# Performance work log

Hardware: AMD Instinct MI355X
Metric: run time of the kernel (lower is better)

Reference implementation:

```python
import jax, jax.numpy as jnp
import numpy as np

B, S, H = 64, 2048, 512


def _xavier(key, shape):
    fan_in, fan_out = shape[-1], shape[-2] if len(shape) > 1 else 1
    limit = float(np.sqrt(6.0 / (fan_in + fan_out)))
    return jax.random.uniform(key, shape, jnp.float32, -limit, limit)


def setup_inputs() -> dict:
    key = jax.random.key(0)
    k1, k2, k3, k4, k5, k6 = jax.random.split(key, 6)
    keys_ = jax.random.normal(k1, (B, S, H), jnp.float32)
    query = jax.random.normal(k2, (B, H), jnp.float32)
    v1 = _xavier(k3, (H,))
    W1 = _xavier(k4, (H, 2 * H))
    v2 = _xavier(k5, (H,))
    W2 = _xavier(k6, (H, 2 * H))
    return {"keys": keys_, "query": query, "v1": v1, "W1": W1, "v2": v2, "W2": W2}


def reference(keys, query, v1, W1, v2, W2):
    b, s, h = keys.shape
    # Stage 1: additive (Bahdanau) scoring over concat(keys, broadcast query)
    q = jnp.broadcast_to(query[:, None, :], (b, s, h))          # [B,S,H]
    hidden = jnp.concatenate([keys, q], axis=2)                  # [B,S,2H]
    t1 = jnp.tanh(jnp.einsum('de,bse->bsd', W1, hidden))         # [B,S,H]
    scores = jnp.einsum('d,bsd->bs', v1, t1)                     # [B,S]
    attns = jax.nn.softmax(scores, axis=1)                       # [B,S]
    # values == keys in the original module
    new_q = jnp.einsum('bs,bsh->bh', attns, keys)                # [B,H]
    # Stage 2: score again against concat(keys, broadcast new_query)
    nq = jnp.broadcast_to(new_q[:, None, :], (b, s, h))
    hidden2 = jnp.concatenate([keys, nq], axis=2)                # [B,S,2H]
    t2 = jnp.tanh(jnp.einsum('de,bse->bsd', W2, hidden2))        # [B,S,H]
    attn_vecs = jnp.einsum('d,bsd->bs', v2, t2)[:, None, :]      # [B,1,S]
    return attn_vecs
```

## Files before the change

kernel.cpp:

```cpp
#include <hip/hip_runtime.h>
#include <cstdint>
#include <cstddef>

#define S_DIM 2048

typedef __attribute__((ext_vector_type(8))) short short8;
typedef __attribute__((ext_vector_type(4))) float f32x4;

static __device__ __forceinline__ unsigned short f2bf(float f) {
  union { float f; unsigned int u; } v; v.f = f;
  unsigned int r = (v.u + 0x7fffu + ((v.u >> 16) & 1u)) >> 16;
  return (unsigned short)r;
}

static __device__ __forceinline__ float bf2f(unsigned short u) {
  union { unsigned int u; float f; } v; v.u = ((unsigned int)u) << 16;
  return v.f;
}

static __device__ __forceinline__ float fast_tanh(float x) {
  x = fminf(15.f, fmaxf(-15.f, x));
  float e = __expf(x + x);
  return 1.f - 2.f * __builtin_amdgcn_rcpf(e + 1.f);
}

static __device__ __forceinline__ void gload_lds16(const void* g, void* l) {
  __builtin_amdgcn_global_load_lds(
      (const __attribute__((address_space(1))) void*)g,
      (__attribute__((address_space(3))) void*)l, 16, 0, 0);
}


__global__ __launch_bounds__(256) void pack_a_kernel(
    const float* __restrict__ keys, unsigned short* __restrict__ akp) {
  int gid = blockIdx.x * 256 + threadIdx.x;
  int tile = gid >> 12;
  int wt = gid & 4095;
  int k0 = wt >> 8, mr = (wt >> 6) & 3, lhi = (wt >> 4) & 3, l15 = wt & 15;
  const float* src = keys + (size_t)(tile * 64 + mr * 16 + l15) * 512 + k0 * 32 + lhi * 8;
  float4 f0 = *reinterpret_cast<const float4*>(src);
  float4 f1 = *reinterpret_cast<const float4*>(src + 4);
  short8 hv;
  hv[0] = (short)f2bf(f0.x); hv[1] = (short)f2bf(f0.y);
  hv[2] = (short)f2bf(f0.z); hv[3] = (short)f2bf(f0.w);
  hv[4] = (short)f2bf(f1.x); hv[5] = (short)f2bf(f1.y);
  hv[6] = (short)f2bf(f1.z); hv[7] = (short)f2bf(f1.w);
  *reinterpret_cast<short8*>(akp + (size_t)gid * 8) = hv;
}

__global__ __launch_bounds__(256) void pack_b_kernel(
    const float* __restrict__ W1, const float* __restrict__ W2,
    unsigned short* __restrict__ wkp1, unsigned short* __restrict__ wkp2) {
  int j = blockIdx.x * 256 + threadIdx.x;
  const float* W = (j < 32768) ? W1 : W2;
  unsigned short* o = (j < 32768) ? wkp1 : wkp2;
  int wt = j & 32767;
  int k0 = wt >> 11, g = (wt >> 6) & 31, lhi = (wt >> 4) & 3, l15 = wt & 15;
  const float* src = W + (size_t)(g * 16 + l15) * 1024 + k0 * 32 + lhi * 8;
  float4 f0 = *reinterpret_cast<const float4*>(src);
  float4 f1 = *reinterpret_cast<const float4*>(src + 4);
  short8 hv;
  hv[0] = (short)f2bf(f0.x); hv[1] = (short)f2bf(f0.y);
  hv[2] = (short)f2bf(f0.z); hv[3] = (short)f2bf(f0.w);
  hv[4] = (short)f2bf(f1.x); hv[5] = (short)f2bf(f1.y);
  hv[6] = (short)f2bf(f1.z); hv[7] = (short)f2bf(f1.w);
  *reinterpret_cast<short8*>(o + (size_t)wt * 8) = hv;
}

__global__ __launch_bounds__(512, 4) void fused_packed_kernel(
    const unsigned short* __restrict__ akp, const unsigned short* __restrict__ wkp,
    const float* __restrict__ v, const float* __restrict__ qp,
    float* __restrict__ out) {
  __shared__ __align__(16) unsigned short lds_a[32768];
  __shared__ float lds_score[8][64];

  const int tid  = threadIdx.x;
  const int wid  = tid >> 6;
  const int lane = tid & 63;
  const int l15  = lane & 15;
  const int lhi  = lane >> 4;
  const int tile = blockIdx.x;
  const int row0 = tile * 64;
  const int b    = row0 >> 11;
  const int wcol = wid * 64;

  const unsigned short* atile = akp + (size_t)tile * 32768;
  #pragma unroll
  for (int i = 0; i < 8; ++i)
    gload_lds16(atile + (i * 512 + tid) * 8, (char*)lds_a + (i * 512 + tid) * 16);

  const unsigned short* wbase = wkp + (size_t)wid * 2048 + (size_t)lane * 8;
  short8 bb[2][4];
  #pragma unroll
  for (int nc = 0; nc < 4; ++nc)
    bb[0][nc] = *reinterpret_cast<const short8*>(wbase + nc * 512);

  __syncthreads();

  f32x4 acc[4][4];
  #pragma unroll
  for (int mr = 0; mr < 4; ++mr)
    #pragma unroll
    for (int nc = 0; nc < 4; ++nc) {
      f32x4 z = {0.f, 0.f, 0.f, 0.f};
      acc[mr][nc] = z;
    }

  const char* abase = (const char*)lds_a + lane * 16;

  #pragma unroll
  for (int k0 = 0; k0 < 16; ++k0) {
    const int cur = k0 & 1, nxt = cur ^ 1;
    if (k0 < 15) {
      #pragma unroll
      for (int nc = 0; nc < 4; ++nc)
        bb[nxt][nc] = *reinterpret_cast<const short8*>(
            wbase + (size_t)(k0 + 1) * 16384 + nc * 512);
    }
    short8 a[4];
    #pragma unroll
    for (int mr = 0; mr < 4; ++mr)
      a[mr] = *reinterpret_cast<const short8*>(abase + k0 * 4096 + mr * 1024);
    #pragma unroll
    for (int mr = 0; mr < 4; ++mr)
      #pragma unroll
      for (int nc = 0; nc < 4; ++nc)
        acc[mr][nc] = __builtin_amdgcn_mfma_f32_16x16x32_bf16(
            a[mr], bb[cur][nc], acc[mr][nc], 0, 0, 0);
  }

  float rp[4][4];
  #pragma unroll
  for (int mr = 0; mr < 4; ++mr)
    #pragma unroll
    for (int j = 0; j < 4; ++j) rp[mr][j] = 0.f;

  #pragma unroll
  for (int nc = 0; nc < 4; ++nc) {
    int col = wcol + nc * 16 + l15;
    float vv = v[col];
    float qv = qp[b * 512 + col];
    #pragma unroll
    for (int mr = 0; mr < 4; ++mr)
      #pragma unroll
      for (int j = 0; j < 4; ++j)
        rp[mr][j] += fast_tanh(acc[mr][nc][j] + qv) * vv;
  }

  #pragma unroll
  for (int off = 1; off < 16; off <<= 1)
    #pragma unroll
    for (int mr = 0; mr < 4; ++mr)
      #pragma unroll
      for (int j = 0; j < 4; ++j)
        rp[mr][j] += __shfl_xor(rp[mr][j], off, 64);

  if (l15 == 0) {
    #pragma unroll
    for (int mr = 0; mr < 4; ++mr)
      #pragma unroll
      for (int j = 0; j < 4; ++j)
        lds_score[wid][mr * 16 + lhi * 4 + j] = rp[mr][j];
  }
  __syncthreads();
  if (tid < 64) {
    float s = 0.f;
    #pragma unroll
    for (int w = 0; w < 8; ++w) s += lds_score[w][tid];
    out[row0 + tid] = s;
  }
}

__global__ __launch_bounds__(256) void wsum_packed_kernel(
    const unsigned short* __restrict__ akp, const float* __restrict__ attn,
    float* __restrict__ new_q) {
  int b = blockIdx.x, k0 = blockIdx.y;
  int t = threadIdx.x;
  int mr = t >> 6, lhi = (t >> 4) & 3, l15 = t & 15;
  const unsigned short* base =
      akp + (size_t)b * 32 * 32768 + (size_t)k0 * 2048 + (size_t)t * 8;
  const float* ab = attn + b * S_DIM + mr * 16 + l15;
  float acc[8];
  #pragma unroll
  for (int e = 0; e < 8; ++e) acc[e] = 0.f;
  #pragma unroll 4
  for (int tile = 0; tile < 32; ++tile) {
    short8 kv = *reinterpret_cast<const short8*>(base + (size_t)tile * 32768);
    float w = ab[tile * 64];
    #pragma unroll
    for (int e = 0; e < 8; ++e)
      acc[e] += w * bf2f((unsigned short)kv[e]);
  }
  __shared__ float red[4][64][8];
  #pragma unroll
  for (int e = 0; e < 8; ++e) red[lhi][mr * 16 + l15][e] = acc[e];
  __syncthreads();
  if (t < 32) {
    int lh = t >> 3, e = t & 7;
    float s = 0.f;
    #pragma unroll 8
    for (int r = 0; r < 64; ++r) s += red[lh][r][e];
    new_q[b * 512 + k0 * 32 + lh * 8 + e] = s;
  }
}


__global__ __launch_bounds__(512) void qproj_kernel(
    const float* __restrict__ W, const float* __restrict__ x,
    float* __restrict__ qp) {
  __shared__ float xs[512];
  int b = blockIdx.x, d = threadIdx.x;
  xs[d] = x[b * 512 + d];
  __syncthreads();
  const float4* wr = (const float4*)(W + (size_t)d * 1024 + 512);
  const float4* xv = (const float4*)xs;
  float acc = 0.f;
  #pragma unroll 8
  for (int h = 0; h < 128; ++h) {
    float4 w4 = wr[h], x4 = xv[h];
    acc += w4.x * x4.x + w4.y * x4.y + w4.z * x4.z + w4.w * x4.w;
  }
  qp[b * 512 + d] = acc;
}

__global__ __launch_bounds__(256) void softmax_kernel(float* __restrict__ sc) {
  int b = blockIdx.x, tid = threadIdx.x;
  float* row = sc + (size_t)b * S_DIM;
  float vv[8];
  float m = -1e30f;
  #pragma unroll
  for (int i = 0; i < 8; ++i) { vv[i] = row[tid + i * 256]; m = fmaxf(m, vv[i]); }
  #pragma unroll
  for (int off = 32; off; off >>= 1) m = fmaxf(m, __shfl_xor(m, off, 64));
  __shared__ float red[4], red2[4];
  int wid = tid >> 6, lane = tid & 63;
  if (lane == 0) red[wid] = m;
  __syncthreads();
  m = fmaxf(fmaxf(red[0], red[1]), fmaxf(red[2], red[3]));
  float s = 0.f;
  #pragma unroll
  for (int i = 0; i < 8; ++i) { vv[i] = __expf(vv[i] - m); s += vv[i]; }
  #pragma unroll
  for (int off = 32; off; off >>= 1) s += __shfl_xor(s, off, 64);
  if (lane == 0) red2[wid] = s;
  __syncthreads();
  s = red2[0] + red2[1] + red2[2] + red2[3];
  float inv = 1.f / s;
  #pragma unroll
  for (int i = 0; i < 8; ++i) row[tid + i * 256] = vv[i] * inv;
}


__global__ __launch_bounds__(256) void convw_kernel(
    const float* __restrict__ W1, const float* __restrict__ W2,
    unsigned short* __restrict__ wk1, unsigned short* __restrict__ wk2) {
  int idx = blockIdx.x * 256 + threadIdx.x;
  const float* W = (idx < 262144) ? W1 : W2;
  unsigned short* o = (idx < 262144) ? wk1 : wk2;
  int j = idx & 262143;
  int d = j >> 9, h = j & 511;
  o[j] = f2bf(W[(size_t)d * 1024 + h]);
}

__global__ __launch_bounds__(512, 4) void fused_scores_kernel(
    const float* __restrict__ keys, const unsigned short* __restrict__ wk,
    const float* __restrict__ v, const float* __restrict__ qp,
    float* __restrict__ out) {
  __shared__ __align__(16) unsigned short lds_k[64 * 512];
  __shared__ float lds_score[8][64];
  char* lds_b = (char*)lds_k;
  const int tid  = threadIdx.x;
  const int wid  = tid >> 6;
  const int lane = tid & 63;
  const int l15  = lane & 15;
  const int lhi  = lane >> 4;
  const int row0 = blockIdx.x * 64;
  const int b    = row0 >> 11;
  const int wcol = wid * 64;
  #pragma unroll
  for (int i = 0; i < 8; ++i) {
    int c = i * 512 + tid;
    int r = c >> 6, k = (c & 63) * 8;
    const float* src = keys + (size_t)(row0 + r) * 512 + k;
    const float4 f0 = *reinterpret_cast<const float4*>(src);
    const float4 f1 = *reinterpret_cast<const float4*>(src + 4);
    short8 hv;
    hv[0] = (short)f2bf(f0.x); hv[1] = (short)f2bf(f0.y);
    hv[2] = (short)f2bf(f0.z); hv[3] = (short)f2bf(f0.w);
    hv[4] = (short)f2bf(f1.x); hv[5] = (short)f2bf(f1.y);
    hv[6] = (short)f2bf(f1.z); hv[7] = (short)f2bf(f1.w);
    int byte = (r * 1024 + k * 2) ^ ((r & 7) << 4);
    *reinterpret_cast<short8*>(lds_b + byte) = hv;
  }
  __syncthreads();
  f32x4 acc[4][4];
  #pragma unroll
  for (int mr = 0; mr < 4; ++mr)
    #pragma unroll
    for (int nc = 0; nc < 4; ++nc) {
      f32x4 z = {0.f, 0.f, 0.f, 0.f};
      acc[mr][nc] = z;
    }
  const int koff = lhi * 8;
  #pragma unroll 1
  for (int k0 = 0; k0 < 512; k0 += 32) {
    short8 a[4], bbv[4];
    #pragma unroll
    for (int nc = 0; nc < 4; ++nc) {
      const unsigned short* p =
          wk + (((size_t)(wcol + nc * 16 + l15)) << 9) + k0 + koff;
      bbv[nc] = *reinterpret_cast<const short8*>(p);
    }
    #pragma unroll
    for (int mr = 0; mr < 4; ++mr) {
      int r = mr * 16 + l15;
      int byte = (r * 1024 + (k0 + koff) * 2) ^ ((r & 7) << 4);
      a[mr] = *reinterpret_cast<const short8*>(lds_b + byte);
    }
    #pragma unroll
    for (int mr = 0; mr < 4; ++mr)
      #pragma unroll
      for (int nc = 0; nc < 4; ++nc)
        acc[mr][nc] = __builtin_amdgcn_mfma_f32_16x16x32_bf16(
            a[mr], bbv[nc], acc[mr][nc], 0, 0, 0);
  }
  float rp[4][4];
  #pragma unroll
  for (int mr = 0; mr < 4; ++mr)
    #pragma unroll
    for (int j = 0; j < 4; ++j) rp[mr][j] = 0.f;
  #pragma unroll
  for (int nc = 0; nc < 4; ++nc) {
    int col = wcol + nc * 16 + l15;
    float vv = v[col];
    float qv = qp[b * 512 + col];
    #pragma unroll
    for (int mr = 0; mr < 4; ++mr)
      #pragma unroll
      for (int j = 0; j < 4; ++j)
        rp[mr][j] += fast_tanh(acc[mr][nc][j] + qv) * vv;
  }
  #pragma unroll
  for (int off = 1; off < 16; off <<= 1)
    #pragma unroll
    for (int mr = 0; mr < 4; ++mr)
      #pragma unroll
      for (int j = 0; j < 4; ++j)
        rp[mr][j] += __shfl_xor(rp[mr][j], off, 64);
  if (l15 == 0) {
    #pragma unroll
    for (int mr = 0; mr < 4; ++mr)
      #pragma unroll
      for (int j = 0; j < 4; ++j)
        lds_score[wid][mr * 16 + lhi * 4 + j] = rp[mr][j];
  }
  __syncthreads();
  if (tid < 64) {
    float s = 0.f;
    #pragma unroll
    for (int w = 0; w < 8; ++w) s += lds_score[w][tid];
    out[row0 + tid] = s;
  }
}

__global__ __launch_bounds__(512) void wsum_part_kernel(
    const float* __restrict__ keys, const float* __restrict__ attn,
    float* __restrict__ part) {
  int b = blockIdx.x, sc = blockIdx.y;
  int tid = threadIdx.x;
  int c4 = tid & 127, rg = tid >> 7;
  const float* kb = keys + ((size_t)(b * S_DIM + sc * 128 + rg * 32)) * 512 + c4 * 4;
  const float* ab = attn + b * S_DIM + sc * 128 + rg * 32;
  float4 acc = {0.f, 0.f, 0.f, 0.f};
  #pragma unroll 8
  for (int i = 0; i < 32; ++i) {
    float w = ab[i];
    float4 kv = *reinterpret_cast<const float4*>(kb + (size_t)i * 512);
    acc.x += w * kv.x; acc.y += w * kv.y; acc.z += w * kv.z; acc.w += w * kv.w;
  }
  __shared__ float4 red[4][128];
  red[rg][c4] = acc;
  __syncthreads();
  if (tid < 128) {
    float4 a0 = red[0][tid], a1 = red[1][tid], a2 = red[2][tid], a3 = red[3][tid];
    float4 s;
    s.x = a0.x + a1.x + a2.x + a3.x;
    s.y = a0.y + a1.y + a2.y + a3.y;
    s.z = a0.z + a1.z + a2.z + a3.z;
    s.w = a0.w + a1.w + a2.w + a3.w;
    *reinterpret_cast<float4*>(part + ((size_t)b * 16 + sc) * 512 + tid * 4) = s;
  }
}

__global__ __launch_bounds__(512) void wsum_final_kernel(
    const float* __restrict__ part, float* __restrict__ new_q) {
  int b = blockIdx.x, h = threadIdx.x;
  float acc = 0.f;
  #pragma unroll
  for (int sc = 0; sc < 16; ++sc) acc += part[((size_t)b * 16 + sc) * 512 + h];
  new_q[b * 512 + h] = acc;
}


extern "C" void kernel_launch(void* const* d_in, const int* in_sizes, int n_in,
                              void* d_out, int out_size, void* d_ws, size_t ws_size,
                              hipStream_t stream) {
  (void)in_sizes; (void)n_in; (void)out_size;
  const float* keys  = (const float*)d_in[0];
  const float* query = (const float*)d_in[1];
  const float* v1    = (const float*)d_in[2];
  const float* W1    = (const float*)d_in[3];
  const float* v2    = (const float*)d_in[4];
  const float* W2    = (const float*)d_in[5];
  float* out = (float*)d_out;
  float* wsf = (float*)d_ws;

  const size_t FAST_NEED = 491520ull * 4ull + 67108864ull * 2ull;
  if (ws_size >= FAST_NEED) {
    float* qp1   = wsf;
    float* attn  = wsf + 32768;
    float* new_q = wsf + 163840;
    float* qp2   = wsf + 196608;
    unsigned short* wkp1 = (unsigned short*)(wsf + 229376);
    unsigned short* wkp2 = wkp1 + 262144;
    unsigned short* akp  = (unsigned short*)(wsf + 491520);

    pack_a_kernel<<<32768, 256, 0, stream>>>(keys, akp);
    pack_b_kernel<<<256, 256, 0, stream>>>(W1, W2, wkp1, wkp2);
    qproj_kernel<<<64, 512, 0, stream>>>(W1, query, qp1);
    fused_packed_kernel<<<2048, 512, 0, stream>>>(akp, wkp1, v1, qp1, attn);
    softmax_kernel<<<64, 256, 0, stream>>>(attn);
    wsum_packed_kernel<<<dim3(64, 16), 256, 0, stream>>>(akp, attn, new_q);
    qproj_kernel<<<64, 512, 0, stream>>>(W2, new_q, qp2);
    fused_packed_kernel<<<2048, 512, 0, stream>>>(akp, wkp2, v2, qp2, out);
  } else {
    float* qp1   = wsf;
    float* attn  = wsf + 32768;
    float* new_q = wsf + 163840;
    float* qp2   = wsf + 196608;
    float* part  = wsf + 229376;
    unsigned short* wk1 = (unsigned short*)(wsf + 753664);
    unsigned short* wk2 = wk1 + 262144;

    convw_kernel<<<2048, 256, 0, stream>>>(W1, W2, wk1, wk2);
    qproj_kernel<<<64, 512, 0, stream>>>(W1, query, qp1);
    fused_scores_kernel<<<2048, 512, 0, stream>>>(keys, wk1, v1, qp1, attn);
    softmax_kernel<<<64, 256, 0, stream>>>(attn);
    wsum_part_kernel<<<dim3(64, 16), 512, 0, stream>>>(keys, attn, part);
    wsum_final_kernel<<<64, 512, 0, stream>>>(part, new_q);
    qproj_kernel<<<64, 512, 0, stream>>>(W2, new_q, qp2);
    fused_scores_kernel<<<2048, 512, 0, stream>>>(keys, wk2, v2, qp2, out);
  }
}
```

Before: 305.0 us.

## Fuse both key projections into one persistent kernel, defer query-dependent tanh

The key half of the W2 projection does not depend on the new query, so a single persistent kernel now computes keys·W1ᵀ and keys·W2ᵀ together. It stages fp32 keys through double-buffered, XOR-swizzled LDS and converts them to bf16 in registers, which removes the separate key packing pass. The W2 partial products are stored as bf16 and a light finisher kernel later adds the projected new query, applies tanh and the v2 dot product. This saves a second full read of keys and a second GEMM, at the cost of writing and rereading a 128 MB bf16 intermediate, using fp32 keys for the weighted sum, and adding some rounding from the bf16 intermediate.

```diff
diff --git a/kernel.cpp b/kernel.cpp
--- a/kernel.cpp
+++ b/kernel.cpp
@@ -18,6 +18,12 @@
   return v.f;
 }
 
+static __device__ __forceinline__ unsigned int cvt_pk_bf16(float lo, float hi) {
+  unsigned int r;
+  asm("v_cvt_pk_bf16_f32 %0, %1, %2" : "=v"(r) : "v"(lo), "v"(hi));
+  return r;
+}
+
 static __device__ __forceinline__ float fast_tanh(float x) {
   x = fminf(15.f, fmaxf(-15.f, x));
   float e = __expf(x + x);
@@ -28,24 +34,6 @@
   __builtin_amdgcn_global_load_lds(
       (const __attribute__((address_space(1))) void*)g,
       (__attribute__((address_space(3))) void*)l, 16, 0, 0);
-}
-
-
-__global__ __launch_bounds__(256) void pack_a_kernel(
-    const float* __restrict__ keys, unsigned short* __restrict__ akp) {
-  int gid = blockIdx.x * 256 + threadIdx.x;
-  int tile = gid >> 12;
-  int wt = gid & 4095;
-  int k0 = wt >> 8, mr = (wt >> 6) & 3, lhi = (wt >> 4) & 3, l15 = wt & 15;
-  const float* src = keys + (size_t)(tile * 64 + mr * 16 + l15) * 512 + k0 * 32 + lhi * 8;
-  float4 f0 = *reinterpret_cast<const float4*>(src);
-  float4 f1 = *reinterpret_cast<const float4*>(src + 4);
-  short8 hv;
-  hv[0] = (short)f2bf(f0.x); hv[1] = (short)f2bf(f0.y);
-  hv[2] = (short)f2bf(f0.z); hv[3] = (short)f2bf(f0.w);
-  hv[4] = (short)f2bf(f1.x); hv[5] = (short)f2bf(f1.y);
-  hv[6] = (short)f2bf(f1.z); hv[7] = (short)f2bf(f1.w);
-  *reinterpret_cast<short8*>(akp + (size_t)gid * 8) = hv;
 }
 
 __global__ __launch_bounds__(256) void pack_b_kernel(
@@ -67,86 +55,186 @@
   *reinterpret_cast<short8*>(o + (size_t)wt * 8) = hv;
 }
 
-__global__ __launch_bounds__(512, 4) void fused_packed_kernel(
-    const unsigned short* __restrict__ akp, const unsigned short* __restrict__ wkp,
-    const float* __restrict__ v, const float* __restrict__ qp,
-    float* __restrict__ out) {
-  __shared__ __align__(16) unsigned short lds_a[32768];
-  __shared__ float lds_score[8][64];
+#define MEGA_K0(CUR, NXT, K0L)                                                 \
+  {                                                                            \
+    if (do_stage) {                                                            \
+      const float* ssrc =                                                      \
+          keys + (size_t)(strow + (K0L) * 8 + wid) * 512 + skb + cs * 4;       \
+      gload_lds16(ssrc,                                                        \
+                  lds_c + (size_t)nbuf * 65536 + ((K0L) * 512 + tid) * 16);    \
+    }                                                                          \
+    if ((K0L) < 7) {                                                           \
+      _Pragma("unroll")                                                        \
+      for (int nc = 0; nc < 8; ++nc)                                           \
+        NXT[nc] = *reinterpret_cast<const short8*>(                            \
+            wb_half + ((K0L) + 1) * 16384 + nc * 512);                         \
+    }                                                                          \
+    _Pragma("unroll")                                                          \
+    for (int mr = 0; mr < 4; ++mr) {                                           \
+      const int r = mr * 16 + l15;                                             \
+      const int tc = (K0L) * 8 + lhi * 2;                                      \
+      const int x = r & 7;                                                     \
+      const char* hb = lds_c + (size_t)half * 65536;                           \
+      f32x4 f0 = *reinterpret_cast<const f32x4*>(                              \
+          hb + r * 1024 + ((tc ^ x) << 4));                                    \
+      f32x4 f1 = *reinterpret_cast<const f32x4*>(                              \
+          hb + r * 1024 + ((((K0L) * 8 + lhi * 2 + 1)) ^ x) * 16);             \
+      union { unsigned int u[4]; short8 s; } av;                               \
+      av.u[0] = cvt_pk_bf16(f0[0], f0[1]);                                     \
+      av.u[1] = cvt_pk_bf16(f0[2], f0[3]);                                     \
+      av.u[2] = cvt_pk_bf16(f1[0], f1[1]);                                     \
+      av.u[3] = cvt_pk_bf16(f1[2], f1[3]);                                     \
+      _Pragma("unroll")                                                        \
+      for (int nc = 0; nc < 8; ++nc)                                           \
+        acc[mr][nc] = __builtin_amdgcn_mfma_f32_16x16x32_bf16(                 \
+            av.s, CUR[nc], acc[mr][nc], 0, 0, 0);                              \
+    }                                                                          \
+  }
+
+__global__ __launch_bounds__(512, 2) void mega_kernel(
+    const float* __restrict__ keys,
+    const unsigned short* __restrict__ wkp1,
+    const unsigned short* __restrict__ wkp2,
+    const float* __restrict__ v1, const float* __restrict__ qp1,
+    float* __restrict__ scores1, unsigned short* __restrict__ p2p) {
+  __shared__ __align__(16) float lds_f[2][64 * 256];
+  __shared__ float lds_score[4][64];
+  char* lds_c = (char*)&lds_f[0][0];
 
   const int tid  = threadIdx.x;
   const int wid  = tid >> 6;
   const int lane = tid & 63;
   const int l15  = lane & 15;
   const int lhi  = lane >> 4;
-  const int tile = blockIdx.x;
-  const int row0 = tile * 64;
-  const int b    = row0 >> 11;
-  const int wcol = wid * 64;
-
-  const unsigned short* atile = akp + (size_t)tile * 32768;
-  #pragma unroll
-  for (int i = 0; i < 8; ++i)
-    gload_lds16(atile + (i * 512 + tid) * 8, (char*)lds_a + (i * 512 + tid) * 16);
-
-  const unsigned short* wbase = wkp + (size_t)wid * 2048 + (size_t)lane * 8;
-  short8 bb[2][4];
-  #pragma unroll
-  for (int nc = 0; nc < 4; ++nc)
-    bb[0][nc] = *reinterpret_cast<const short8*>(wbase + nc * 512);
-
-  __syncthreads();
-
-  f32x4 acc[4][4];
+  const int bid  = blockIdx.x;
+  const int strip = wid & 3;
+  const bool isW2 = wid >= 4;
+  const unsigned short* wkp = isW2 ? wkp2 : wkp1;
+  const unsigned short* wbase = wkp + (size_t)strip * 4096 + (size_t)lane * 8;
+  const int cs = lane ^ wid;
+
+  {
+    const int trow = bid * 512;
+    #pragma unroll
+    for (int k0l = 0; k0l < 8; ++k0l) {
+      const float* ssrc = keys + (size_t)(trow + k0l * 8 + wid) * 512 + cs * 4;
+      gload_lds16(ssrc, lds_c + ((k0l * 512 + tid) * 16));
+    }
+  }
+  __syncthreads();
+
+  #pragma unroll 1
+  for (int it = 0; it < 8; ++it) {
+    const int tile = bid * 8 + it;
+    const int row0 = tile * 64;
+    const int b    = row0 >> 11;
+
+    f32x4 acc[4][8];
+    #pragma unroll
+    for (int mr = 0; mr < 4; ++mr)
+      #pragma unroll
+      for (int nc = 0; nc < 8; ++nc) {
+        f32x4 z = {0.f, 0.f, 0.f, 0.f};
+        acc[mr][nc] = z;
+      }
+
+    #pragma unroll
+    for (int half = 0; half < 2; ++half) {
+      const bool do_stage = (half == 0) || (it < 7);
+      const int strow = (half == 0) ? row0 : (row0 + 64);
+      const int skb   = (half == 0) ? 256 : 0;
+      const int nbuf  = half ^ 1;
+      const unsigned short* wb_half = wbase + (size_t)half * 8 * 16384;
+
+      short8 b0[8], b1[8];
+      #pragma unroll
+      for (int nc = 0; nc < 8; ++nc)
+        b0[nc] = *reinterpret_cast<const short8*>(wb_half + nc * 512);
+
+      MEGA_K0(b0, b1, 0) MEGA_K0(b1, b0, 1) MEGA_K0(b0, b1, 2) MEGA_K0(b1, b0, 3)
+      MEGA_K0(b0, b1, 4) MEGA_K0(b1, b0, 5) MEGA_K0(b0, b1, 6) MEGA_K0(b1, b0, 7)
+      __syncthreads();
+    }
+
+    if (!isW2) {
+      float rp[4][4];
+      #pragma unroll
+      for (int mr = 0; mr < 4; ++mr)
+        #pragma unroll
+        for (int j = 0; j < 4; ++j) rp[mr][j] = 0.f;
+      #pragma unroll
+      for (int nc = 0; nc < 8; ++nc) {
+        const int col = strip * 128 + nc * 16 + l15;
+        const float vv = v1[col];
+        const float qv = qp1[b * 512 + col];
+        #pragma unroll
+        for (int mr = 0; mr < 4; ++mr)
+          #pragma unroll
+          for (int j = 0; j < 4; ++j)
+            rp[mr][j] += fast_tanh(acc[mr][nc][j] + qv) * vv;
+      }
+      #pragma unroll
+      for (int off = 1; off < 16; off <<= 1)
+        #pragma unroll
+        for (int mr = 0; mr < 4; ++mr)
+          #pragma unroll
+          for (int j = 0; j < 4; ++j)
+            rp[mr][j] += __shfl_xor(rp[mr][j], off, 64);
+      if (l15 == 0) {
+        #pragma unroll
+        for (int mr = 0; mr < 4; ++mr)
+          #pragma unroll
+          for (int j = 0; j < 4; ++j)
+            lds_score[wid][mr * 16 + lhi * 4 + j] = rp[mr][j];
+      }
+    } else {
+      unsigned short* pt = p2p + (size_t)tile * 32768;
+      #pragma unroll
+      for (int mr = 0; mr < 4; ++mr)
+        #pragma unroll
+        for (int nc = 0; nc < 8; ++nc) {
+          union { unsigned int u[2]; ushort4 s; } o;
+          o.u[0] = cvt_pk_bf16(acc[mr][nc][0], acc[mr][nc][1]);
+          o.u[1] = cvt_pk_bf16(acc[mr][nc][2], acc[mr][nc][3]);
+          *reinterpret_cast<ushort4*>(
+              pt + (size_t)((strip * 32 + mr * 8 + nc) * 64 + lane) * 4) = o.s;
+        }
+    }
+    __syncthreads();
+    if (tid < 64)
+      scores1[row0 + tid] = lds_score[0][tid] + lds_score[1][tid] +
+                            lds_score[2][tid] + lds_score[3][tid];
+  }
+}
+
+__global__ __launch_bounds__(256) void finisher_kernel(
+    const unsigned short* __restrict__ p2p, const float* __restrict__ v2,
+    const float* __restrict__ qp2, float* __restrict__ out) {
+  __shared__ float lds_score[4][64];
+  const int tid = threadIdx.x, wi = tid >> 6, lane = tid & 63;
+  const int l15 = lane & 15, lhi = lane >> 4;
+  const int tile = blockIdx.x, row0 = tile * 64, b = row0 >> 11;
+  const unsigned short* pt = p2p + (size_t)tile * 32768;
+  float rp[4][4];
   #pragma unroll
   for (int mr = 0; mr < 4; ++mr)
     #pragma unroll
-    for (int nc = 0; nc < 4; ++nc) {
-      f32x4 z = {0.f, 0.f, 0.f, 0.f};
-      acc[mr][nc] = z;
-    }
-
-  const char* abase = (const char*)lds_a + lane * 16;
-
-  #pragma unroll
-  for (int k0 = 0; k0 < 16; ++k0) {
-    const int cur = k0 & 1, nxt = cur ^ 1;
-    if (k0 < 15) {
-      #pragma unroll
-      for (int nc = 0; nc < 4; ++nc)
-        bb[nxt][nc] = *reinterpret_cast<const short8*>(
-            wbase + (size_t)(k0 + 1) * 16384 + nc * 512);
-    }
-    short8 a[4];
-    #pragma unroll
-    for (int mr = 0; mr < 4; ++mr)
-      a[mr] = *reinterpret_cast<const short8*>(abase + k0 * 4096 + mr * 1024);
-    #pragma unroll
-    for (int mr = 0; mr < 4; ++mr)
-      #pragma unroll
-      for (int nc = 0; nc < 4; ++nc)
-        acc[mr][nc] = __builtin_amdgcn_mfma_f32_16x16x32_bf16(
-            a[mr], bb[cur][nc], acc[mr][nc], 0, 0, 0);
-  }
-
-  float rp[4][4];
-  #pragma unroll
-  for (int mr = 0; mr < 4; ++mr)
-    #pragma unroll
     for (int j = 0; j < 4; ++j) rp[mr][j] = 0.f;
-
-  #pragma unroll
-  for (int nc = 0; nc < 4; ++nc) {
-    int col = wcol + nc * 16 + l15;
-    float vv = v[col];
-    float qv = qp[b * 512 + col];
-    #pragma unroll
-    for (int mr = 0; mr < 4; ++mr)
-      #pragma unroll
-      for (int j = 0; j < 4; ++j)
-        rp[mr][j] += fast_tanh(acc[mr][nc][j] + qv) * vv;
-  }
-
+  #pragma unroll
+  for (int nc = 0; nc < 8; ++nc) {
+    const int col = wi * 128 + nc * 16 + l15;
+    const float vv = v2[col];
+    const float qv = qp2[b * 512 + col];
+    #pragma unroll
+    for (int mr = 0; mr < 4; ++mr) {
+      ushort4 pv = *reinterpret_cast<const ushort4*>(
+          pt + (size_t)((wi * 32 + mr * 8 + nc) * 64 + lane) * 4);
+      rp[mr][0] += fast_tanh(bf2f(pv.x) + qv) * vv;
+      rp[mr][1] += fast_tanh(bf2f(pv.y) + qv) * vv;
+      rp[mr][2] += fast_tanh(bf2f(pv.z) + qv) * vv;
+      rp[mr][3] += fast_tanh(bf2f(pv.w) + qv) * vv;
+    }
+  }
   #pragma unroll
   for (int off = 1; off < 16; off <<= 1)
     #pragma unroll
@@ -154,54 +242,17 @@
       #pragma unroll
       for (int j = 0; j < 4; ++j)
         rp[mr][j] += __shfl_xor(rp[mr][j], off, 64);
-
   if (l15 == 0) {
     #pragma unroll
     for (int mr = 0; mr < 4; ++mr)
       #pragma unroll
       for (int j = 0; j < 4; ++j)
-        lds_score[wid][mr * 16 + lhi * 4 + j] = rp[mr][j];
-  }
-  __syncthreads();
-  if (tid < 64) {
-    float s = 0.f;
-    #pragma unroll
-    for (int w = 0; w < 8; ++w) s += lds_score[w][tid];
-    out[row0 + tid] = s;
-  }
-}
-
-__global__ __launch_bounds__(256) void wsum_packed_kernel(
-    const unsigned short* __restrict__ akp, const float* __restrict__ attn,
-    float* __restrict__ new_q) {
-  int b = blockIdx.x, k0 = blockIdx.y;
-  int t = threadIdx.x;
-  int mr = t >> 6, lhi = (t >> 4) & 3, l15 = t & 15;
-  const unsigned short* base =
-      akp + (size_t)b * 32 * 32768 + (size_t)k0 * 2048 + (size_t)t * 8;
-  const float* ab = attn + b * S_DIM + mr * 16 + l15;
-  float acc[8];
-  #pragma unroll
-  for (int e = 0; e < 8; ++e) acc[e] = 0.f;
-  #pragma unroll 4
-  for (int tile = 0; tile < 32; ++tile) {
-    short8 kv = *reinterpret_cast<const short8*>(base + (size_t)tile * 32768);
-    float w = ab[tile * 64];
-    #pragma unroll
-    for (int e = 0; e < 8; ++e)
-      acc[e] += w * bf2f((unsigned short)kv[e]);
-  }
-  __shared__ float red[4][64][8];
-  #pragma unroll
-  for (int e = 0; e < 8; ++e) red[lhi][mr * 16 + l15][e] = acc[e];
-  __syncthreads();
-  if (t < 32) {
-    int lh = t >> 3, e = t & 7;
-    float s = 0.f;
-    #pragma unroll 8
-    for (int r = 0; r < 64; ++r) s += red[lh][r][e];
-    new_q[b * 512 + k0 * 32 + lh * 8 + e] = s;
-  }
+        lds_score[wi][mr * 16 + lhi * 4 + j] = rp[mr][j];
+  }
+  __syncthreads();
+  if (tid < 64)
+    out[row0 + tid] = lds_score[0][tid] + lds_score[1][tid] +
+                      lds_score[2][tid] + lds_score[3][tid];
 }
 
 
@@ -248,6 +299,44 @@
   float inv = 1.f / s;
   #pragma unroll
   for (int i = 0; i < 8; ++i) row[tid + i * 256] = vv[i] * inv;
+}
+
+__global__ __launch_bounds__(512) void wsum_part_kernel(
+    const float* __restrict__ keys, const float* __restrict__ attn,
+    float* __restrict__ part) {
+  int b = blockIdx.x, sc = blockIdx.y;
+  int tid = threadIdx.x;
+  int c4 = tid & 127, rg = tid >> 7;
+  const float* kb = keys + ((size_t)(b * S_DIM + sc * 128 + rg * 32)) * 512 + c4 * 4;
+  const float* ab = attn + b * S_DIM + sc * 128 + rg * 32;
+  float4 acc = {0.f, 0.f, 0.f, 0.f};
+  #pragma unroll 8
+  for (int i = 0; i < 32; ++i) {
+    float w = ab[i];
+    float4 kv = *reinterpret_cast<const float4*>(kb + (size_t)i * 512);
+    acc.x += w * kv.x; acc.y += w * kv.y; acc.z += w * kv.z; acc.w += w * kv.w;
+  }
+  __shared__ float4 red[4][128];
+  red[rg][c4] = acc;
+  __syncthreads();
+  if (tid < 128) {
+    float4 a0 = red[0][tid], a1 = red[1][tid], a2 = red[2][tid], a3 = red[3][tid];
+    float4 s;
+    s.x = a0.x + a1.x + a2.x + a3.x;
+    s.y = a0.y + a1.y + a2.y + a3.y;
+    s.z = a0.z + a1.z + a2.z + a3.z;
+    s.w = a0.w + a1.w + a2.w + a3.w;
+    *reinterpret_cast<float4*>(part + ((size_t)b * 16 + sc) * 512 + tid * 4) = s;
+  }
+}
+
+__global__ __launch_bounds__(512) void wsum_final_kernel(
+    const float* __restrict__ part, float* __restrict__ new_q) {
+  int b = blockIdx.x, h = threadIdx.x;
+  float acc = 0.f;
+  #pragma unroll
+  for (int sc = 0; sc < 16; ++sc) acc += part[((size_t)b * 16 + sc) * 512 + h];
+  new_q[b * 512 + h] = acc;
 }
 
 
@@ -363,44 +452,6 @@
   }
 }
 
-__global__ __launch_bounds__(512) void wsum_part_kernel(
-    const float* __restrict__ keys, const float* __restrict__ attn,
-    float* __restrict__ part) {
-  int b = blockIdx.x, sc = blockIdx.y;
-  int tid = threadIdx.x;
-  int c4 = tid & 127, rg = tid >> 7;
-  const float* kb = keys + ((size_t)(b * S_DIM + sc * 128 + rg * 32)) * 512 + c4 * 4;
-  const float* ab = attn + b * S_DIM + sc * 128 + rg * 32;
-  float4 acc = {0.f, 0.f, 0.f, 0.f};
-  #pragma unroll 8
-  for (int i = 0; i < 32; ++i) {
-    float w = ab[i];
-    float4 kv = *reinterpret_cast<const float4*>(kb + (size_t)i * 512);
-    acc.x += w * kv.x; acc.y += w * kv.y; acc.z += w * kv.z; acc.w += w * kv.w;
-  }
-  __shared__ float4 red[4][128];
-  red[rg][c4] = acc;
-  __syncthreads();
-  if (tid < 128) {
-    float4 a0 = red[0][tid], a1 = red[1][tid], a2 = red[2][tid], a3 = red[3][tid];
-    float4 s;
-    s.x = a0.x + a1.x + a2.x + a3.x;
-    s.y = a0.y + a1.y + a2.y + a3.y;
-    s.z = a0.z + a1.z + a2.z + a3.z;
-    s.w = a0.w + a1.w + a2.w + a3.w;
-    *reinterpret_cast<float4*>(part + ((size_t)b * 16 + sc) * 512 + tid * 4) = s;
-  }
-}
-
-__global__ __launch_bounds__(512) void wsum_final_kernel(
-    const float* __restrict__ part, float* __restrict__ new_q) {
-  int b = blockIdx.x, h = threadIdx.x;
-  float acc = 0.f;
-  #pragma unroll
-  for (int sc = 0; sc < 16; ++sc) acc += part[((size_t)b * 16 + sc) * 512 + h];
-  new_q[b * 512 + h] = acc;
-}
-
 
 extern "C" void kernel_launch(void* const* d_in, const int* in_sizes, int n_in,
                               void* d_out, int out_size, void* d_ws, size_t ws_size,
@@ -415,24 +466,25 @@
   float* out = (float*)d_out;
   float* wsf = (float*)d_ws;
 
-  const size_t FAST_NEED = 491520ull * 4ull + 67108864ull * 2ull;
+  const size_t FAST_NEED = 34570240ull * 4ull;
   if (ws_size >= FAST_NEED) {
     float* qp1   = wsf;
     float* attn  = wsf + 32768;
     float* new_q = wsf + 163840;
     float* qp2   = wsf + 196608;
-    unsigned short* wkp1 = (unsigned short*)(wsf + 229376);
+    float* part  = wsf + 229376;
+    unsigned short* wkp1 = (unsigned short*)(wsf + 753664);
     unsigned short* wkp2 = wkp1 + 262144;
-    unsigned short* akp  = (unsigned short*)(wsf + 491520);
-
-    pack_a_kernel<<<32768, 256, 0, stream>>>(keys, akp);
+    unsigned short* p2p  = (unsigned short*)(wsf + 1015808);
+
     pack_b_kernel<<<256, 256, 0, stream>>>(W1, W2, wkp1, wkp2);
     qproj_kernel<<<64, 512, 0, stream>>>(W1, query, qp1);
-    fused_packed_kernel<<<2048, 512, 0, stream>>>(akp, wkp1, v1, qp1, attn);
+    mega_kernel<<<256, 512, 0, stream>>>(keys, wkp1, wkp2, v1, qp1, attn, p2p);
     softmax_kernel<<<64, 256, 0, stream>>>(attn);
-    wsum_packed_kernel<<<dim3(64, 16), 256, 0, stream>>>(akp, attn, new_q);
+    wsum_part_kernel<<<dim3(64, 16), 512, 0, stream>>>(keys, attn, part);
+    wsum_final_kernel<<<64, 512, 0, stream>>>(part, new_q);
     qproj_kernel<<<64, 512, 0, stream>>>(W2, new_q, qp2);
-    fused_packed_kernel<<<2048, 512, 0, stream>>>(akp, wkp2, v2, qp2, out);
+    finisher_kernel<<<2048, 256, 0, stream>>>(p2p, v2, qp2, out);
   } else {
     float* qp1   = wsf;
     float* attn  = wsf + 32768;
```

Measured after the change: 752.3 us. +146.7%, slower.

## Use 128-row tiles with triple-buffered LDS staging of A and W in GEMM

Applied to the files above, without the earlier changes.

Replaces the 64-row fused scoring kernel with a 128-row kernel that streams both the packed keys and the packed weight slices through a three-stage LDS ring via direct global-to-LDS loads. It uses explicit waitcnt and barriers plus setprio around the MFMA bursts. Each block now reuses every weight fragment across twice as many rows, and weight loads move from per-wave registers into shared LDS. The pack_a kernel is rewritten to read keys contiguously and scatter its writes, and it is launched after the small pack/qproj kernels. The kernel allows fewer blocks per CU and depends on hand-tuned vmcnt counts.

```diff
diff --git a/kernel.cpp b/kernel.cpp
--- a/kernel.cpp
+++ b/kernel.cpp
@@ -30,14 +30,20 @@
       (__attribute__((address_space(3))) void*)l, 16, 0, 0);
 }
 
+#define VMW(N) asm volatile("s_waitcnt vmcnt(" #N ")" ::: "memory")
+#define LGK0() asm volatile("s_waitcnt lgkmcnt(0)" ::: "memory")
+#define BAR()  __builtin_amdgcn_s_barrier()
+
 
 __global__ __launch_bounds__(256) void pack_a_kernel(
     const float* __restrict__ keys, unsigned short* __restrict__ akp) {
   int gid = blockIdx.x * 256 + threadIdx.x;
-  int tile = gid >> 12;
-  int wt = gid & 4095;
-  int k0 = wt >> 8, mr = (wt >> 6) & 3, lhi = (wt >> 4) & 3, l15 = wt & 15;
-  const float* src = keys + (size_t)(tile * 64 + mr * 16 + l15) * 512 + k0 * 32 + lhi * 8;
+  size_t e = (size_t)gid * 8;
+  int r = (int)(e >> 9), k = (int)(e & 511);
+  int t = r >> 6, rl = r & 63;
+  int mr = rl >> 4, l15 = rl & 15;
+  int k0 = k >> 5, lhi = (k >> 3) & 3;
+  const float* src = keys + e;
   float4 f0 = *reinterpret_cast<const float4*>(src);
   float4 f1 = *reinterpret_cast<const float4*>(src + 4);
   short8 hv;
@@ -45,7 +51,8 @@
   hv[2] = (short)f2bf(f0.z); hv[3] = (short)f2bf(f0.w);
   hv[4] = (short)f2bf(f1.x); hv[5] = (short)f2bf(f1.y);
   hv[6] = (short)f2bf(f1.z); hv[7] = (short)f2bf(f1.w);
-  *reinterpret_cast<short8*>(akp + (size_t)gid * 8) = hv;
+  size_t wt = (size_t)k0 * 256 + mr * 64 + lhi * 16 + l15;
+  *reinterpret_cast<short8*>(akp + (size_t)t * 32768 + wt * 8) = hv;
 }
 
 __global__ __launch_bounds__(256) void pack_b_kernel(
@@ -67,103 +74,121 @@
   *reinterpret_cast<short8*>(o + (size_t)wt * 8) = hv;
 }
 
-__global__ __launch_bounds__(512, 4) void fused_packed_kernel(
+__global__ __launch_bounds__(512, 2) void gemm8p_kernel(
     const unsigned short* __restrict__ akp, const unsigned short* __restrict__ wkp,
     const float* __restrict__ v, const float* __restrict__ qp,
     float* __restrict__ out) {
-  __shared__ __align__(16) unsigned short lds_a[32768];
-  __shared__ float lds_score[8][64];
+  __shared__ __align__(16) char lds_stage[3][40960];
+  __shared__ float lds_score[8][128];
 
   const int tid  = threadIdx.x;
   const int wid  = tid >> 6;
   const int lane = tid & 63;
   const int l15  = lane & 15;
   const int lhi  = lane >> 4;
-  const int tile = blockIdx.x;
-  const int row0 = tile * 64;
+  const int w4   = wid * 4;
+  const int blk  = blockIdx.x;
+  const int row0 = blk * 128;
   const int b    = row0 >> 11;
-  const int wcol = wid * 64;
-
-  const unsigned short* atile = akp + (size_t)tile * 32768;
-  #pragma unroll
-  for (int i = 0; i < 8; ++i)
-    gload_lds16(atile + (i * 512 + tid) * 8, (char*)lds_a + (i * 512 + tid) * 16);
-
-  const unsigned short* wbase = wkp + (size_t)wid * 2048 + (size_t)lane * 8;
-  short8 bb[2][4];
-  #pragma unroll
-  for (int nc = 0; nc < 4; ++nc)
-    bb[0][nc] = *reinterpret_cast<const short8*>(wbase + nc * 512);
-
-  __syncthreads();
-
-  f32x4 acc[4][4];
-  #pragma unroll
-  for (int mr = 0; mr < 4; ++mr)
+  const unsigned short* at0 = akp + (size_t)(blk * 2) * 32768;
+  const unsigned short* at1 = at0 + 32768;
+  const int ai = wid * 5;
+
+#define G8_STAGE(I) do {                                                     \
+    char* dst_ = &lds_stage[(I) % 3][ai * 1024];                             \
+    _Pragma("unroll")                                                        \
+    for (int q_ = 0; q_ < 5; ++q_) {                                         \
+      const int a_ = ai + q_;                                                \
+      const unsigned short* src_;                                            \
+      if (a_ < 4)      src_ = at0 + (I) * 2048 + a_ * 512;                   \
+      else if (a_ < 8) src_ = at1 + (I) * 2048 + (a_ - 4) * 512;             \
+      else             src_ = wkp + (size_t)(I) * 16384 + (a_ - 8) * 512;    \
+      gload_lds16(src_ + lane * 8, dst_ + q_ * 1024);                        \
+    }                                                                        \
+  } while (0)
+
+#define G8_COMPUTE(I) do {                                                   \
+    const char* bs_ = lds_stage[(I) % 3];                                    \
+    short8 a_[8], bf_[4];                                                    \
+    _Pragma("unroll")                                                        \
+    for (int mr = 0; mr < 8; ++mr)                                           \
+      a_[mr] = *reinterpret_cast<const short8*>(                             \
+          bs_ + (mr >> 2) * 4096 + ((mr & 3) * 64 + lane) * 16);             \
+    _Pragma("unroll")                                                        \
+    for (int nc = 0; nc < 4; ++nc)                                           \
+      bf_[nc] = *reinterpret_cast<const short8*>(                            \
+          bs_ + 8192 + ((w4 + nc) * 64 + lane) * 16);                        \
+    __builtin_amdgcn_s_setprio(1);                                           \
+    _Pragma("unroll")                                                        \
+    for (int mr = 0; mr < 8; ++mr)                                           \
+      _Pragma("unroll")                                                      \
+      for (int nc = 0; nc < 4; ++nc)                                         \
+        acc[mr][nc] = __builtin_amdgcn_mfma_f32_16x16x32_bf16(               \
+            a_[mr], bf_[nc], acc[mr][nc], 0, 0, 0);                          \
+    __builtin_amdgcn_s_setprio(0);                                           \
+  } while (0)
+
+#define G8_FULL(I) do {                                                      \
+    G8_COMPUTE(I); LGK0(); BAR();                                            \
+    G8_STAGE((I) + 3); VMW(10); BAR();                                       \
+  } while (0)
+
+  f32x4 acc[8][4];
+  #pragma unroll
+  for (int mr = 0; mr < 8; ++mr)
     #pragma unroll
     for (int nc = 0; nc < 4; ++nc) {
       f32x4 z = {0.f, 0.f, 0.f, 0.f};
       acc[mr][nc] = z;
     }
 
-  const char* abase = (const char*)lds_a + lane * 16;
-
-  #pragma unroll
-  for (int k0 = 0; k0 < 16; ++k0) {
-    const int cur = k0 & 1, nxt = cur ^ 1;
-    if (k0 < 15) {
-      #pragma unroll
-      for (int nc = 0; nc < 4; ++nc)
-        bb[nxt][nc] = *reinterpret_cast<const short8*>(
-            wbase + (size_t)(k0 + 1) * 16384 + nc * 512);
-    }
-    short8 a[4];
-    #pragma unroll
-    for (int mr = 0; mr < 4; ++mr)
-      a[mr] = *reinterpret_cast<const short8*>(abase + k0 * 4096 + mr * 1024);
-    #pragma unroll
-    for (int mr = 0; mr < 4; ++mr)
-      #pragma unroll
-      for (int nc = 0; nc < 4; ++nc)
-        acc[mr][nc] = __builtin_amdgcn_mfma_f32_16x16x32_bf16(
-            a[mr], bb[cur][nc], acc[mr][nc], 0, 0, 0);
-  }
-
-  float rp[4][4];
-  #pragma unroll
-  for (int mr = 0; mr < 4; ++mr)
+  G8_STAGE(0); G8_STAGE(1); G8_STAGE(2);
+  VMW(10); BAR();
+
+  G8_FULL(0);  G8_FULL(1);  G8_FULL(2);  G8_FULL(3);
+  G8_FULL(4);  G8_FULL(5);  G8_FULL(6);  G8_FULL(7);
+  G8_FULL(8);  G8_FULL(9);  G8_FULL(10); G8_FULL(11);
+  G8_FULL(12);
+  G8_COMPUTE(13); LGK0(); BAR(); VMW(5); BAR();
+  G8_COMPUTE(14); LGK0(); BAR(); VMW(0); BAR();
+  G8_COMPUTE(15);
+
+#undef G8_FULL
+#undef G8_COMPUTE
+#undef G8_STAGE
+
+  float rp[8][4];
+  #pragma unroll
+  for (int mr = 0; mr < 8; ++mr)
     #pragma unroll
     for (int j = 0; j < 4; ++j) rp[mr][j] = 0.f;
-
   #pragma unroll
   for (int nc = 0; nc < 4; ++nc) {
-    int col = wcol + nc * 16 + l15;
-    float vv = v[col];
-    float qv = qp[b * 512 + col];
-    #pragma unroll
-    for (int mr = 0; mr < 4; ++mr)
+    const int col = wid * 64 + nc * 16 + l15;
+    const float vv = v[col];
+    const float qv = qp[b * 512 + col];
+    #pragma unroll
+    for (int mr = 0; mr < 8; ++mr)
       #pragma unroll
       for (int j = 0; j < 4; ++j)
         rp[mr][j] += fast_tanh(acc[mr][nc][j] + qv) * vv;
   }
-
   #pragma unroll
   for (int off = 1; off < 16; off <<= 1)
     #pragma unroll
-    for (int mr = 0; mr < 4; ++mr)
+    for (int mr = 0; mr < 8; ++mr)
       #pragma unroll
       for (int j = 0; j < 4; ++j)
         rp[mr][j] += __shfl_xor(rp[mr][j], off, 64);
-
   if (l15 == 0) {
     #pragma unroll
-    for (int mr = 0; mr < 4; ++mr)
+    for (int mr = 0; mr < 8; ++mr)
       #pragma unroll
       for (int j = 0; j < 4; ++j)
         lds_score[wid][mr * 16 + lhi * 4 + j] = rp[mr][j];
   }
   __syncthreads();
-  if (tid < 64) {
+  if (tid < 128) {
     float s = 0.f;
     #pragma unroll
     for (int w = 0; w < 8; ++w) s += lds_score[w][tid];
@@ -425,14 +450,14 @@
     unsigned short* wkp2 = wkp1 + 262144;
     unsigned short* akp  = (unsigned short*)(wsf + 491520);
 
-    pack_a_kernel<<<32768, 256, 0, stream>>>(keys, akp);
     pack_b_kernel<<<256, 256, 0, stream>>>(W1, W2, wkp1, wkp2);
     qproj_kernel<<<64, 512, 0, stream>>>(W1, query, qp1);
-    fused_packed_kernel<<<2048, 512, 0, stream>>>(akp, wkp1, v1, qp1, attn);
+    pack_a_kernel<<<32768, 256, 0, stream>>>(keys, akp);
+    gemm8p_kernel<<<1024, 512, 0, stream>>>(akp, wkp1, v1, qp1, attn);
     softmax_kernel<<<64, 256, 0, stream>>>(attn);
     wsum_packed_kernel<<<dim3(64, 16), 256, 0, stream>>>(akp, attn, new_q);
     qproj_kernel<<<64, 512, 0, stream>>>(W2, new_q, qp2);
-    fused_packed_kernel<<<2048, 512, 0, stream>>>(akp, wkp2, v2, qp2, out);
+    gemm8p_kernel<<<1024, 512, 0, stream>>>(akp, wkp2, v2, qp2, out);
   } else {
     float* qp1   = wsf;
     float* attn  = wsf + 32768;
```

Measured after the change: 397.7 us. 30.4% more time.
